# Kernel optimization log

Hardware: AMD Instinct MI355X
Metric: run time of the kernel (lower is better)

The kernel has to match this reference:

```python
import jax, jax.numpy as jnp
import numpy as np

P = 9  # patch_size


def setup_inputs() -> dict:
    key = jax.random.key(0)
    k1, k2 = jax.random.split(key)
    x = jax.random.normal(k1, (1, 4, 72, 72, 72), dtype=jnp.float32)
    # L = (72//9) * ((72*72)//9) = 8 * 576 = 4608
    attentions = jax.random.normal(k2, (1, 4, 4608, 4608), dtype=jnp.float32)
    return {"x": x, "attentions": attentions}


def reference(x, attentions):
    B, C, D, H, W = x.shape  # B == 1
    Hp, Wp = D, H * W
    x4 = x.reshape(1, C, Hp, Wp)  # [1, C, 72, 5184]
    nH, nW = Hp // P, Wp // P
    L = nH * nW

    # unfold (im2col), stride == kernel so it's a pure reshape/transpose:
    # cols[c, ki*P+kj, bi*nW+bj] = x4[0, c, bi*P+ki, bj*P+kj]
    patches = (
        x4[0]
        .reshape(C, nH, P, nW, P)
        .transpose(0, 2, 4, 1, 3)  # [C, P, P, nH, nW]
        .reshape(C, P * P, L)
    )

    attn = attentions[0]  # [C, L, L]
    # count_nonzero normalization (boolean mask -> no grad path, matches torch)
    nz = jnp.sum(attn != 0, axis=-1).astype(x.dtype)[..., None] + 1e-5  # [C, L, 1]
    attn_norm = attn / nz

    # att[c, l, k] = sum_m attn_norm[c, l, m] * patches[c, k, m]
    att = jnp.einsum("clm,ckm->clk", attn_norm, patches)  # [C, L, P*P]

    # fold (col2im), stride == kernel: inverse reshape/transpose
    corr = (
        att.transpose(0, 2, 1)  # [C, P*P, L]
        .reshape(C, P, P, nH, nW)
        .transpose(0, 3, 1, 4, 2)  # [C, nH, P, nW, P]
        .reshape(C, Hp, Wp)
    )[None]  # [1, C, Hp, Wp]

    out = corr * x4 + x4
    return jax.nn.leaky_relu(out, negative_slope=0.2)
```

## Files before the change

### kernel.cpp

```cpp
#include <hip/hip_runtime.h>
#include <hip/hip_bf16.h>
#include <stdint.h>

#define PSZ    9
#define CH     4
#define LROWS  4608
#define NWp    576
#define HPdim  72
#define WPdim  5184
#define NPAD   96
#define NVALID 81
#define KSPLIT 4
#define KSEG   (LROWS / KSPLIT)
#define KBLK   32
#define NKB    (LROWS / KBLK)
#define BCH    (NPAD * KBLK)

typedef short s16x8 __attribute__((ext_vector_type(8)));
typedef float f32x4 __attribute__((ext_vector_type(4)));

__device__ __forceinline__ uint16_t f2bf(float f) {
    uint32_t u = __builtin_bit_cast(uint32_t, f);
    u += 0x8000u;
    return (uint16_t)(u >> 16);
}

__device__ __forceinline__ s16x8 cvt8(float4 a, float4 b) {
    union { s16x8 v; uint32_t u[4]; } r;
    __hip_bfloat162 h0 = __float22bfloat162_rn(make_float2(a.x, a.y));
    __hip_bfloat162 h1 = __float22bfloat162_rn(make_float2(a.z, a.w));
    __hip_bfloat162 h2 = __float22bfloat162_rn(make_float2(b.x, b.y));
    __hip_bfloat162 h3 = __float22bfloat162_rn(make_float2(b.z, b.w));
    __builtin_memcpy(&r.u[0], &h0, 4);
    __builtin_memcpy(&r.u[1], &h1, 4);
    __builtin_memcpy(&r.u[2], &h2, 4);
    __builtin_memcpy(&r.u[3], &h3, 4);
    return r.v;
}

__device__ __forceinline__ int count8(float4 a, float4 b) {
    return (a.x != 0.f) + (a.y != 0.f) + (a.z != 0.f) + (a.w != 0.f)
         + (b.x != 0.f) + (b.y != 0.f) + (b.z != 0.f) + (b.w != 0.f);
}

__global__ __launch_bounds__(256) void build_pb_kernel(
    const float* __restrict__ x, uint16_t* __restrict__ pb)
{
    __shared__ float xs[PSZ][288];
    const int blk = blockIdx.x;
    const int c   = blk / NKB;
    const int kb  = blk - c * NKB;
    const int bi  = kb / 18;
    const int bj0 = (kb - bi * 18) * KBLK;

    const float* src = x + (size_t)(c * HPdim + bi * PSZ) * WPdim + bj0 * PSZ;
    for (int idx = threadIdx.x; idx < PSZ * 288; idx += 256) {
        int r = idx / 288, col = idx - r * 288;
        xs[r][col] = src[(size_t)r * WPdim + col];
    }
    __syncthreads();

    uint16_t* dst = pb + (size_t)(c * NKB + kb) * BCH;
    for (int oidx = threadIdx.x; oidx < BCH; oidx += 256) {
        int n = oidx / KBLK, ks = oidx - n * KBLK;
        uint16_t v = 0;
        if (n < NVALID) {
            int ki = n / PSZ, kj = n - ki * PSZ;
            v = f2bf(xs[ki][ks * PSZ + kj]);
        }
        dst[oidx] = v;
    }
}

__global__ __launch_bounds__(256) void cross_gemm_kernel(
    const float* __restrict__ x,
    const float* __restrict__ attn,
    const uint16_t* __restrict__ pb,
    float* __restrict__ out)
{
    __shared__ float red[KSPLIT - 1][64][25];
    __shared__ int   cshared[KSPLIT][16];

    const int lane = threadIdx.x & 63;
    const int widx = threadIdx.x >> 6;
    const int blk  = blockIdx.x;
    const int slot = blk & 7;
    const int ii   = blk >> 3;
    const int c    = slot >> 1;
    const int tile = (slot & 1) * 144 + ii;
    const int r0   = tile * 16;
    const int li   = lane & 15;
    const int quad = lane >> 4;
    const int k0   = widx * KSEG;
    const int kb0  = k0 / KBLK;

    const float* ap = attn + (size_t)(c * LROWS + r0 + li) * LROWS + k0 + quad * 8;
    const uint16_t* bp = pb + (size_t)(c * NKB + kb0) * BCH + li * KBLK + quad * 8;

    f32x4 acc[6];
#pragma unroll
    for (int t = 0; t < 6; ++t) acc[t] = (f32x4){0.f, 0.f, 0.f, 0.f};

    int cnt = 0;
    const int DITERS = KSEG / 64;

    float4 a00 = *(const float4*)(ap);
    float4 a01 = *(const float4*)(ap + 4);
    s16x8 b0[6];
#pragma unroll
    for (int t = 0; t < 6; ++t) b0[t] = *(const s16x8*)(bp + t * 16 * KBLK);

    for (int dit = 0; dit < DITERS - 1; ++dit) {
        float4 a10 = *(const float4*)(ap + 32);
        float4 a11 = *(const float4*)(ap + 36);
        s16x8 b1[6];
#pragma unroll
        for (int t = 0; t < 6; ++t) b1[t] = *(const s16x8*)(bp + BCH + t * 16 * KBLK);

        cnt += count8(a00, a01);
        {
            s16x8 af = cvt8(a00, a01);
#pragma unroll
            for (int t = 0; t < 6; ++t)
                acc[t] = __builtin_amdgcn_mfma_f32_16x16x32_bf16(af, b0[t], acc[t], 0, 0, 0);
        }

        ap += 64;
        bp += 2 * BCH;
        a00 = *(const float4*)(ap);
        a01 = *(const float4*)(ap + 4);
#pragma unroll
        for (int t = 0; t < 6; ++t) b0[t] = *(const s16x8*)(bp + t * 16 * KBLK);

        cnt += count8(a10, a11);
        {
            s16x8 af = cvt8(a10, a11);
#pragma unroll
            for (int t = 0; t < 6; ++t)
                acc[t] = __builtin_amdgcn_mfma_f32_16x16x32_bf16(af, b1[t], acc[t], 0, 0, 0);
        }
    }

    {
        float4 a10 = *(const float4*)(ap + 32);
        float4 a11 = *(const float4*)(ap + 36);
        s16x8 b1[6];
#pragma unroll
        for (int t = 0; t < 6; ++t) b1[t] = *(const s16x8*)(bp + BCH + t * 16 * KBLK);

        cnt += count8(a00, a01);
        {
            s16x8 af = cvt8(a00, a01);
#pragma unroll
            for (int t = 0; t < 6; ++t)
                acc[t] = __builtin_amdgcn_mfma_f32_16x16x32_bf16(af, b0[t], acc[t], 0, 0, 0);
        }
        cnt += count8(a10, a11);
        {
            s16x8 af = cvt8(a10, a11);
#pragma unroll
            for (int t = 0; t < 6; ++t)
                acc[t] = __builtin_amdgcn_mfma_f32_16x16x32_bf16(af, b1[t], acc[t], 0, 0, 0);
        }
    }

    cnt += __shfl_down(cnt, 32);
    cnt += __shfl_down(cnt, 16);
    if (lane < 16) cshared[widx][lane] = cnt;

    if (widx > 0) {
#pragma unroll
        for (int t = 0; t < 6; ++t)
#pragma unroll
            for (int r = 0; r < 4; ++r)
                red[widx - 1][lane][t * 4 + r] = acc[t][r];
    }
    __syncthreads();

    if (widx == 0) {
#pragma unroll
        for (int reg = 0; reg < 4; ++reg) {
            const int lrow = quad * 4 + reg;
            const int cnt_r = cshared[0][lrow] + cshared[1][lrow]
                            + cshared[2][lrow] + cshared[3][lrow];
            const float scale = 1.0f / ((float)cnt_r + 1e-5f);
            const int l  = r0 + lrow;
            const int bi = l / NWp;
            const int bj = l - bi * NWp;
#pragma unroll
            for (int t = 0; t < 6; ++t) {
                const int n = t * 16 + li;
                if (n < NVALID) {
                    const float v = acc[t][reg]
                                  + red[0][lane][t * 4 + reg]
                                  + red[1][lane][t * 4 + reg]
                                  + red[2][lane][t * 4 + reg];
                    const int ki = n / PSZ, kj = n - (n / PSZ) * PSZ;
                    const size_t idx = (size_t)(c * HPdim + bi * PSZ + ki) * WPdim
                                     + (size_t)(bj * PSZ + kj);
                    const float xv = x[idx];
                    const float o  = xv * (1.0f + v * scale);
                    out[idx] = (o > 0.f) ? o : 0.2f * o;
                }
            }
        }
    }
}

extern "C" void kernel_launch(void* const* d_in, const int* in_sizes, int n_in,
                              void* d_out, int out_size, void* d_ws, size_t ws_size,
                              hipStream_t stream)
{
    const float* x    = (const float*)d_in[0];
    const float* attn = (const float*)d_in[1];
    float* out        = (float*)d_out;
    uint16_t* pb      = (uint16_t*)d_ws;

    build_pb_kernel<<<CH * NKB, 256, 0, stream>>>(x, pb);
    cross_gemm_kernel<<<CH * 288, 256, 0, stream>>>(x, attn, pb, out);
}
```

Measured before the change: 502.9 us.

## Process four 16-row groups per workgroup to reuse B fragments

Each workgroup now computes 64 output rows (four 16-row groups) instead of 16, so each loaded B fragment from the packed patch buffer feeds four times as many MFMAs. The grid shrinks by four and the split-K reduction is done in two shared-memory passes with a padded layout. This cuts redundant B loads through L2 at the cost of more registers per thread, fewer workgroups for latency hiding, and possible spilling.

```diff
diff --git a/kernel.cpp b/kernel.cpp
--- a/kernel.cpp
+++ b/kernel.cpp
@@ -72,14 +72,14 @@
     }
 }
 
-__global__ __launch_bounds__(256) void cross_gemm_kernel(
+__global__ __launch_bounds__(256, 2) void cross_gemm_kernel(
     const float* __restrict__ x,
     const float* __restrict__ attn,
     const uint16_t* __restrict__ pb,
     float* __restrict__ out)
 {
-    __shared__ float red[KSPLIT - 1][64][25];
-    __shared__ int   cshared[KSPLIT][16];
+    __shared__ float red[2][KSPLIT - 1][64][26];
+    __shared__ int   cshared[4][KSPLIT][16];
 
     const int lane = threadIdx.x & 63;
     const int widx = threadIdx.x >> 6;
@@ -87,120 +87,170 @@
     const int slot = blk & 7;
     const int ii   = blk >> 3;
     const int c    = slot >> 1;
-    const int tile = (slot & 1) * 144 + ii;
-    const int r0   = tile * 16;
+    const int tile = (slot & 1) * 36 + ii;
+    const int r0   = tile * 64;
     const int li   = lane & 15;
     const int quad = lane >> 4;
     const int k0   = widx * KSEG;
     const int kb0  = k0 / KBLK;
 
-    const float* ap = attn + (size_t)(c * LROWS + r0 + li) * LROWS + k0 + quad * 8;
+    const float* ap[4];
+#pragma unroll
+    for (int g = 0; g < 4; ++g)
+        ap[g] = attn + (size_t)(c * LROWS + r0 + g * 16 + li) * LROWS + k0 + quad * 8;
     const uint16_t* bp = pb + (size_t)(c * NKB + kb0) * BCH + li * KBLK + quad * 8;
 
-    f32x4 acc[6];
-#pragma unroll
-    for (int t = 0; t < 6; ++t) acc[t] = (f32x4){0.f, 0.f, 0.f, 0.f};
-
-    int cnt = 0;
+    f32x4 acc[4][6];
+#pragma unroll
+    for (int g = 0; g < 4; ++g)
+#pragma unroll
+        for (int t = 0; t < 6; ++t) acc[g][t] = (f32x4){0.f, 0.f, 0.f, 0.f};
+
+    int cnt[4] = {0, 0, 0, 0};
     const int DITERS = KSEG / 64;
 
-    float4 a00 = *(const float4*)(ap);
-    float4 a01 = *(const float4*)(ap + 4);
+    float4 a0[4][2];
+#pragma unroll
+    for (int g = 0; g < 4; ++g) {
+        a0[g][0] = *(const float4*)(ap[g]);
+        a0[g][1] = *(const float4*)(ap[g] + 4);
+    }
     s16x8 b0[6];
 #pragma unroll
     for (int t = 0; t < 6; ++t) b0[t] = *(const s16x8*)(bp + t * 16 * KBLK);
 
     for (int dit = 0; dit < DITERS - 1; ++dit) {
-        float4 a10 = *(const float4*)(ap + 32);
-        float4 a11 = *(const float4*)(ap + 36);
+        float4 a1[4][2];
+#pragma unroll
+        for (int g = 0; g < 4; ++g) {
+            a1[g][0] = *(const float4*)(ap[g] + 32);
+            a1[g][1] = *(const float4*)(ap[g] + 36);
+        }
         s16x8 b1[6];
 #pragma unroll
         for (int t = 0; t < 6; ++t) b1[t] = *(const s16x8*)(bp + BCH + t * 16 * KBLK);
 
-        cnt += count8(a00, a01);
-        {
-            s16x8 af = cvt8(a00, a01);
-#pragma unroll
-            for (int t = 0; t < 6; ++t)
-                acc[t] = __builtin_amdgcn_mfma_f32_16x16x32_bf16(af, b0[t], acc[t], 0, 0, 0);
-        }
-
-        ap += 64;
+#pragma unroll
+        for (int g = 0; g < 4; ++g) {
+            cnt[g] += count8(a0[g][0], a0[g][1]);
+            s16x8 af = cvt8(a0[g][0], a0[g][1]);
+#pragma unroll
+            for (int t = 0; t < 6; ++t)
+                acc[g][t] = __builtin_amdgcn_mfma_f32_16x16x32_bf16(af, b0[t], acc[g][t], 0, 0, 0);
+        }
+
+#pragma unroll
+        for (int g = 0; g < 4; ++g) ap[g] += 64;
         bp += 2 * BCH;
-        a00 = *(const float4*)(ap);
-        a01 = *(const float4*)(ap + 4);
+#pragma unroll
+        for (int g = 0; g < 4; ++g) {
+            a0[g][0] = *(const float4*)(ap[g]);
+            a0[g][1] = *(const float4*)(ap[g] + 4);
+        }
 #pragma unroll
         for (int t = 0; t < 6; ++t) b0[t] = *(const s16x8*)(bp + t * 16 * KBLK);
 
-        cnt += count8(a10, a11);
-        {
-            s16x8 af = cvt8(a10, a11);
-#pragma unroll
-            for (int t = 0; t < 6; ++t)
-                acc[t] = __builtin_amdgcn_mfma_f32_16x16x32_bf16(af, b1[t], acc[t], 0, 0, 0);
+#pragma unroll
+        for (int g = 0; g < 4; ++g) {
+            cnt[g] += count8(a1[g][0], a1[g][1]);
+            s16x8 af = cvt8(a1[g][0], a1[g][1]);
+#pragma unroll
+            for (int t = 0; t < 6; ++t)
+                acc[g][t] = __builtin_amdgcn_mfma_f32_16x16x32_bf16(af, b1[t], acc[g][t], 0, 0, 0);
         }
     }
 
     {
-        float4 a10 = *(const float4*)(ap + 32);
-        float4 a11 = *(const float4*)(ap + 36);
+        float4 a1[4][2];
+#pragma unroll
+        for (int g = 0; g < 4; ++g) {
+            a1[g][0] = *(const float4*)(ap[g] + 32);
+            a1[g][1] = *(const float4*)(ap[g] + 36);
+        }
         s16x8 b1[6];
 #pragma unroll
         for (int t = 0; t < 6; ++t) b1[t] = *(const s16x8*)(bp + BCH + t * 16 * KBLK);
 
-        cnt += count8(a00, a01);
-        {
-            s16x8 af = cvt8(a00, a01);
-#pragma unroll
-            for (int t = 0; t < 6; ++t)
-                acc[t] = __builtin_amdgcn_mfma_f32_16x16x32_bf16(af, b0[t], acc[t], 0, 0, 0);
-        }
-        cnt += count8(a10, a11);
-        {
-            s16x8 af = cvt8(a10, a11);
-#pragma unroll
-            for (int t = 0; t < 6; ++t)
-                acc[t] = __builtin_amdgcn_mfma_f32_16x16x32_bf16(af, b1[t], acc[t], 0, 0, 0);
-        }
-    }
-
-    cnt += __shfl_down(cnt, 32);
-    cnt += __shfl_down(cnt, 16);
-    if (lane < 16) cshared[widx][lane] = cnt;
-
-    if (widx > 0) {
-#pragma unroll
-        for (int t = 0; t < 6; ++t)
-#pragma unroll
-            for (int r = 0; r < 4; ++r)
-                red[widx - 1][lane][t * 4 + r] = acc[t][r];
-    }
-    __syncthreads();
-
-    if (widx == 0) {
-#pragma unroll
-        for (int reg = 0; reg < 4; ++reg) {
-            const int lrow = quad * 4 + reg;
-            const int cnt_r = cshared[0][lrow] + cshared[1][lrow]
-                            + cshared[2][lrow] + cshared[3][lrow];
-            const float scale = 1.0f / ((float)cnt_r + 1e-5f);
-            const int l  = r0 + lrow;
-            const int bi = l / NWp;
-            const int bj = l - bi * NWp;
-#pragma unroll
-            for (int t = 0; t < 6; ++t) {
-                const int n = t * 16 + li;
-                if (n < NVALID) {
-                    const float v = acc[t][reg]
-                                  + red[0][lane][t * 4 + reg]
-                                  + red[1][lane][t * 4 + reg]
-                                  + red[2][lane][t * 4 + reg];
-                    const int ki = n / PSZ, kj = n - (n / PSZ) * PSZ;
-                    const size_t idx = (size_t)(c * HPdim + bi * PSZ + ki) * WPdim
-                                     + (size_t)(bj * PSZ + kj);
-                    const float xv = x[idx];
-                    const float o  = xv * (1.0f + v * scale);
-                    out[idx] = (o > 0.f) ? o : 0.2f * o;
+#pragma unroll
+        for (int g = 0; g < 4; ++g) {
+            cnt[g] += count8(a0[g][0], a0[g][1]);
+            s16x8 af = cvt8(a0[g][0], a0[g][1]);
+#pragma unroll
+            for (int t = 0; t < 6; ++t)
+                acc[g][t] = __builtin_amdgcn_mfma_f32_16x16x32_bf16(af, b0[t], acc[g][t], 0, 0, 0);
+        }
+#pragma unroll
+        for (int g = 0; g < 4; ++g) {
+            cnt[g] += count8(a1[g][0], a1[g][1]);
+            s16x8 af = cvt8(a1[g][0], a1[g][1]);
+#pragma unroll
+            for (int t = 0; t < 6; ++t)
+                acc[g][t] = __builtin_amdgcn_mfma_f32_16x16x32_bf16(af, b1[t], acc[g][t], 0, 0, 0);
+        }
+    }
+
+#pragma unroll
+    for (int g = 0; g < 4; ++g) {
+        cnt[g] += __shfl_down(cnt[g], 32);
+        cnt[g] += __shfl_down(cnt[g], 16);
+    }
+    if (lane < 16) {
+#pragma unroll
+        for (int g = 0; g < 4; ++g) cshared[g][widx][lane] = cnt[g];
+    }
+
+#pragma unroll
+    for (int p = 0; p < 2; ++p) {
+        const int s0 = 2 * p, s1 = 2 * p + 1;
+        if (p) __syncthreads();
+
+        if (widx != s0) {
+            const int j = widx - (widx > s0 ? 1 : 0);
+#pragma unroll
+            for (int t = 0; t < 6; ++t)
+#pragma unroll
+                for (int r = 0; r < 4; ++r)
+                    red[0][j][lane][t * 4 + r] = acc[s0][t][r];
+        }
+        if (widx != s1) {
+            const int j = widx - (widx > s1 ? 1 : 0);
+#pragma unroll
+            for (int t = 0; t < 6; ++t)
+#pragma unroll
+                for (int r = 0; r < 4; ++r)
+                    red[1][j][lane][t * 4 + r] = acc[s1][t][r];
+        }
+        __syncthreads();
+
+#pragma unroll
+        for (int h = 0; h < 2; ++h) {
+            const int s = 2 * p + h;
+            if (widx == s) {
+#pragma unroll
+                for (int reg = 0; reg < 4; ++reg) {
+                    const int lrow = quad * 4 + reg;
+                    const int cnt_r = cshared[s][0][lrow] + cshared[s][1][lrow]
+                                    + cshared[s][2][lrow] + cshared[s][3][lrow];
+                    const float scale = 1.0f / ((float)cnt_r + 1e-5f);
+                    const int l  = r0 + s * 16 + lrow;
+                    const int bi = l / NWp;
+                    const int bj = l - bi * NWp;
+#pragma unroll
+                    for (int t = 0; t < 6; ++t) {
+                        const int n = t * 16 + li;
+                        if (n < NVALID) {
+                            const float v = acc[s][t][reg]
+                                          + red[h][0][lane][t * 4 + reg]
+                                          + red[h][1][lane][t * 4 + reg]
+                                          + red[h][2][lane][t * 4 + reg];
+                            const int ki = n / PSZ, kj = n - (n / PSZ) * PSZ;
+                            const size_t idx = (size_t)(c * HPdim + bi * PSZ + ki) * WPdim
+                                             + (size_t)(bj * PSZ + kj);
+                            const float xv = x[idx];
+                            const float o  = xv * (1.0f + v * scale);
+                            out[idx] = (o > 0.f) ? o : 0.2f * o;
+                        }
+                    }
                 }
             }
         }
@@ -217,5 +267,5 @@
     uint16_t* pb      = (uint16_t*)d_ws;
 
     build_pb_kernel<<<CH * NKB, 256, 0, stream>>>(x, pb);
-    cross_gemm_kernel<<<CH * 288, 256, 0, stream>>>(x, attn, pb, out);
-}
+    cross_gemm_kernel<<<CH * 72, 256, 0, stream>>>(x, attn, pb, out);
+}
```

Measured after the change: 509.4 us. Within noise of the previous version (+1.3%).
